# Optimization experiments

Hardware: AMD Instinct MI355X
Metric: run time of the kernel (lower is better)

The kernel has to match this reference:

```python
import jax, jax.numpy as jnp
import numpy as np


def setup_inputs() -> dict:
    key = jax.random.key(0)
    ks = jax.random.split(key, 8)
    B, N, H = 8, 64, 256
    nE, E = 256, 64
    HID, OUT = 512, 1
    s1 = 1.0 / np.sqrt(H + E)
    s2 = 1.0 / np.sqrt(HID)
    return {
        "h_all": jax.random.normal(ks[0], (B, N, H), dtype=jnp.float32),
        "e_feat": jax.random.normal(ks[1], (nE, E), dtype=jnp.float32),
        "W1": jax.random.normal(ks[2], (H + E, HID), dtype=jnp.float32) * s1,
        "b1": jnp.zeros((HID,), dtype=jnp.float32),
        "W2": jax.random.normal(ks[3], (HID, HID), dtype=jnp.float32) * s2,
        "b2": jnp.zeros((HID,), dtype=jnp.float32),
        "W3": jax.random.normal(ks[4], (HID, OUT), dtype=jnp.float32) * s2,
        "b3": jnp.zeros((OUT,), dtype=jnp.float32),
    }


def reference(h_all, e_feat, W1, b1, W2, b2, W3, b3):
    # Math == MLP(cat([expand(h), expand(e)], -1)) but computed via split
    # weights: cat([h,e]) @ W1 == h @ W1[:H] + e @ W1[H:], avoiding the
    # materialized [B,N,nE,H+E] concat tensor.
    H = h_all.shape[-1]
    Wh, We = W1[:H], W1[H:]
    h_part = jnp.einsum("bnh,hk->bnk", h_all, Wh)        # [B,N,HID]
    e_part = jnp.einsum("ed,dk->ek", e_feat, We)          # [nE,HID]
    x = h_part[:, :, None, :] + e_part[None, None, :, :] + b1  # [B,N,nE,HID]
    x = jax.nn.relu(x)
    x = jax.nn.relu(jnp.einsum("bnek,kj->bnej", x, W2) + b2)
    return jnp.einsum("bnek,ko->bneo", x, W3) + b3        # [B,N,nE,OUT]
```

## Files before the change

kernel.cpp:

```cpp
#include <hip/hip_runtime.h>
#include <hip/hip_bf16.h>
#include <hip/hip_fp16.h>


typedef __attribute__((ext_vector_type(8))) _Float16 f16x8;
typedef __attribute__((ext_vector_type(4))) float f32x4;

static __device__ __forceinline__ ushort2 pk_f16(float a, float b) {
  union { __half2 h; ushort2 u; } c;
  c.h = __float22half2_rn(make_float2(a, b));
  return c.u;
}

__global__ __launch_bounds__(256) void k_prep(
    const float* __restrict__ h_all, const float* __restrict__ e_feat,
    const float* __restrict__ W1, const float* __restrict__ b1,
    const float* __restrict__ W2,
    unsigned short* __restrict__ hpb, unsigned short* __restrict__ epb,
    unsigned short* __restrict__ w2f) {
  __shared__ float sm[64 * 68];
  const int t = threadIdx.x;
  const int b = blockIdx.x;

  if (b < 256) {
    const int r0 = b * 2;
    float (*hs)[256] = (float(*)[256])sm;
    hs[0][t] = h_all[(size_t)r0 * 256 + t];
    hs[1][t] = h_all[(size_t)(r0 + 1) * 256 + t];
    __syncthreads();
    float2 a0 = make_float2(0.f, 0.f), a1 = make_float2(0.f, 0.f);
    #pragma unroll 2
    for (int k = 0; k < 256; k += 4) {
      float2 w0 = *(const float2*)(W1 + (size_t)k * 512 + 2 * t);
      float2 w1 = *(const float2*)(W1 + (size_t)(k + 1) * 512 + 2 * t);
      float2 w2v = *(const float2*)(W1 + (size_t)(k + 2) * 512 + 2 * t);
      float2 w3v = *(const float2*)(W1 + (size_t)(k + 3) * 512 + 2 * t);
      float h00 = hs[0][k], h01 = hs[0][k + 1], h02 = hs[0][k + 2], h03 = hs[0][k + 3];
      float h10 = hs[1][k], h11 = hs[1][k + 1], h12 = hs[1][k + 2], h13 = hs[1][k + 3];
      a0.x = fmaf(h00, w0.x, a0.x); a0.y = fmaf(h00, w0.y, a0.y);
      a1.x = fmaf(h10, w0.x, a1.x); a1.y = fmaf(h10, w0.y, a1.y);
      a0.x = fmaf(h01, w1.x, a0.x); a0.y = fmaf(h01, w1.y, a0.y);
      a1.x = fmaf(h11, w1.x, a1.x); a1.y = fmaf(h11, w1.y, a1.y);
      a0.x = fmaf(h02, w2v.x, a0.x); a0.y = fmaf(h02, w2v.y, a0.y);
      a1.x = fmaf(h12, w2v.x, a1.x); a1.y = fmaf(h12, w2v.y, a1.y);
      a0.x = fmaf(h03, w3v.x, a0.x); a0.y = fmaf(h03, w3v.y, a0.y);
      a1.x = fmaf(h13, w3v.x, a1.x); a1.y = fmaf(h13, w3v.y, a1.y);
    }
    float2 bv = *(const float2*)(b1 + 2 * t);
    *(ushort2*)(hpb + (size_t)r0 * 512 + 2 * t) = pk_f16(a0.x + bv.x, a0.y + bv.y);
    *(ushort2*)(hpb + (size_t)(r0 + 1) * 512 + 2 * t) = pk_f16(a1.x + bv.x, a1.y + bv.y);
  } else if (b < 288) {
    const int r0 = (b - 256) * 8;
    sm[t] = e_feat[(size_t)r0 * 64 + t];
    sm[256 + t] = e_feat[(size_t)r0 * 64 + 256 + t];
    __syncthreads();
    float2 acc[8];
    #pragma unroll
    for (int i = 0; i < 8; ++i) acc[i] = make_float2(0.f, 0.f);
    for (int k = 0; k < 64; ++k) {
      float2 wv = *(const float2*)(W1 + (size_t)(256 + k) * 512 + 2 * t);
      #pragma unroll
      for (int i = 0; i < 8; ++i) {
        acc[i].x = fmaf(sm[i * 64 + k], wv.x, acc[i].x);
        acc[i].y = fmaf(sm[i * 64 + k], wv.y, acc[i].y);
      }
    }
    #pragma unroll
    for (int i = 0; i < 8; ++i)
      *(ushort2*)(epb + (size_t)(r0 + i) * 512 + 2 * t) = pk_f16(acc[i].x, acc[i].y);
  } else {
    const int bb = b - 288;
    const int k0 = (bb >> 3) * 64;
    const int c0 = (bb & 7) * 64;
    #pragma unroll
    for (int rr = 0; rr < 4; ++rr) {
      const int row = rr * 16 + (t >> 4);
      float4 v = *(const float4*)(W2 + (size_t)(k0 + row) * 512 + c0 + (t & 15) * 4);
      *(float4*)(&sm[row * 68 + (t & 15) * 4]) = v;
    }
    __syncthreads();
    #pragma unroll
    for (int s2 = 0; s2 < 2; ++s2) {
      const int s = t * 2 + s2;
      const int rec = s >> 6, l = s & 63;
      const int jg = (c0 >> 4) + (rec & 3);
      const int ksg = (k0 >> 5) + (rec >> 2);
      const int cl = (rec & 3) * 16 + (l & 15);
      const int kl = (rec >> 2) * 32 + (l >> 4) * 8;
      union { ushort2 o[4]; uint4 v; } u;
      #pragma unroll
      for (int uu = 0; uu < 4; ++uu)
        u.o[uu] = pk_f16(sm[(kl + 2 * uu) * 68 + cl], sm[(kl + 2 * uu + 1) * 68 + cl]);
      *(uint4*)(w2f + ((size_t)(jg * 16 + ksg) * 64 + l) * 8) = u.v;
    }
  }
}

__global__ __launch_bounds__(256, 2) void k_main(
    const unsigned short* __restrict__ hpb, const unsigned short* __restrict__ epb,
    const unsigned short* __restrict__ w2f, const float* __restrict__ b2,
    const float* __restrict__ W3, const float* __restrict__ b3,
    float* __restrict__ out) {
  __shared__ unsigned short x1s[64 * 512];

  const int t = threadIdx.x;
  const int lane = t & 63;
  const int w = t >> 6;
  const int l15 = lane & 15, l4 = lane >> 4;
  const int bn = blockIdx.x >> 2;
  const int e0 = (blockIdx.x & 3) << 6;
  const int off = (blockIdx.x * 11) & 15;
  const unsigned short* hprow = hpb + (size_t)bn * 512;

  const unsigned short* wrec = w2f + (size_t)w * 65536 + (size_t)lane * 8;
  f16x8 bb[2][8];
  #pragma unroll
  for (int j = 0; j < 8; ++j) {
    bb[0][j] = *(const f16x8*)(wrec + j * 8192 + (size_t)off * 512);
    bb[1][j] = *(const f16x8*)(wrec + j * 8192 + (size_t)((off + 1) & 15) * 512);
  }

  {
    const int kk = t & 63;
    const int rbase = t >> 6;
    const f16x8 fz = {0, 0, 0, 0, 0, 0, 0, 0};
    const f16x8 hv = *(const f16x8*)(hprow + kk * 8);
    #pragma unroll 2
    for (int rr = 0; rr < 16; ++rr) {
      const int r = rr * 4 + rbase;
      f16x8 ev = *(const f16x8*)(epb + (size_t)(e0 + r) * 512 + kk * 8);
      f16x8 x = hv + ev;
      x = __builtin_elementwise_max(x, fz);
      *(f16x8*)(&x1s[r * 512 + (kk ^ (r & 7)) * 8]) = x;
    }
  }
  __syncthreads();

  f32x4 acc[4][8] = {};
  #pragma unroll 2
  for (int ks = 0; ks < 14; ++ks) {
    const int cur = ks & 1;
    const int kr = (ks + off) & 15;
    const int krb = (ks + 2 + off) & 15;
    f16x8 a[4];
    #pragma unroll
    for (int i = 0; i < 4; ++i) {
      const int r = i * 16 + l15;
      a[i] = *(const f16x8*)(&x1s[r * 512 + (((kr * 4 + l4) ^ (l15 & 7)) * 8)]);
    }
    __builtin_amdgcn_s_setprio(1);
    #pragma unroll
    for (int i = 0; i < 4; ++i)
      #pragma unroll
      for (int j = 0; j < 8; ++j)
        acc[i][j] = __builtin_amdgcn_mfma_f32_16x16x32_f16(a[i], bb[cur][j], acc[i][j], 0, 0, 0);
    __builtin_amdgcn_s_setprio(0);
    #pragma unroll
    for (int j = 0; j < 8; ++j)
      bb[cur][j] = *(const f16x8*)(wrec + j * 8192 + (size_t)krb * 512);
  }
  #pragma unroll
  for (int ks = 14; ks < 16; ++ks) {
    const int cur = ks & 1;
    const int kr = (ks + off) & 15;
    f16x8 a[4];
    #pragma unroll
    for (int i = 0; i < 4; ++i) {
      const int r = i * 16 + l15;
      a[i] = *(const f16x8*)(&x1s[r * 512 + (((kr * 4 + l4) ^ (l15 & 7)) * 8)]);
    }
    __builtin_amdgcn_s_setprio(1);
    #pragma unroll
    for (int i = 0; i < 4; ++i)
      #pragma unroll
      for (int j = 0; j < 8; ++j)
        acc[i][j] = __builtin_amdgcn_mfma_f32_16x16x32_f16(a[i], bb[cur][j], acc[i][j], 0, 0, 0);
    __builtin_amdgcn_s_setprio(0);
  }

  float part[16];
  #pragma unroll
  for (int u = 0; u < 16; ++u) part[u] = 0.f;
  #pragma unroll
  for (int j = 0; j < 8; ++j) {
    const int n = w * 128 + j * 16 + l15;
    const float b2v = b2[n], w3v = W3[n];
    #pragma unroll
    for (int i = 0; i < 4; ++i)
      #pragma unroll
      for (int r = 0; r < 4; ++r)
        part[i * 4 + r] = fmaf(fmaxf(acc[i][j][r] + b2v, 0.f), w3v, part[i * 4 + r]);
  }
  #pragma unroll
  for (int u = 0; u < 16; ++u) {
    float v = part[u];
    v += __shfl_xor(v, 1);
    v += __shfl_xor(v, 2);
    v += __shfl_xor(v, 4);
    v += __shfl_xor(v, 8);
    part[u] = v;
  }
  __syncthreads();
  float* osum = (float*)x1s;
  if (l15 == 0) {
    #pragma unroll
    for (int i = 0; i < 4; ++i)
      #pragma unroll
      for (int r = 0; r < 4; ++r)
        osum[w * 64 + i * 16 + l4 * 4 + r] = part[i * 4 + r];
  }
  __syncthreads();
  if (t < 64) {
    float s = b3[0] + osum[t] + osum[64 + t] + osum[128 + t] + osum[192 + t];
    out[(size_t)bn * 256 + e0 + t] = s;
  }
}

extern "C" void kernel_launch(void* const* d_in, const int* in_sizes, int n_in,
                              void* d_out, int out_size, void* d_ws, size_t ws_size,
                              hipStream_t stream) {
  const float* h_all  = (const float*)d_in[0];
  const float* e_feat = (const float*)d_in[1];
  const float* W1     = (const float*)d_in[2];
  const float* b1     = (const float*)d_in[3];
  const float* W2     = (const float*)d_in[4];
  const float* b2     = (const float*)d_in[5];
  const float* W3     = (const float*)d_in[6];
  const float* b3     = (const float*)d_in[7];
  float* out = (float*)d_out;

  unsigned short* hpb = (unsigned short*)d_ws;
  unsigned short* epb = hpb + 512 * 512;
  unsigned short* w2f = epb + 256 * 512;

  hipLaunchKernelGGL(k_prep, dim3(352), dim3(256), 0, stream,
                     h_all, e_feat, W1, b1, W2, hpb, epb, w2f);
  hipLaunchKernelGGL(k_main, dim3(2048), dim3(256), 0, stream,
                     hpb, epb, w2f, b2, W3, b3, out);
}
```

Measured before the change: 140.7 us.

## Switch second-layer GEMM to 32x32x16 MFMA with matching W2 fragment layout

```diff
diff --git a/kernel.cpp b/kernel.cpp
--- a/kernel.cpp
+++ b/kernel.cpp
@@ -4,7 +4,7 @@
 
 
 typedef __attribute__((ext_vector_type(8))) _Float16 f16x8;
-typedef __attribute__((ext_vector_type(4))) float f32x4;
+typedef __attribute__((ext_vector_type(16))) float f32x16;
 
 static __device__ __forceinline__ ushort2 pk_f16(float a, float b) {
   union { __half2 h; ushort2 u; } c;
@@ -69,9 +69,9 @@
     for (int i = 0; i < 8; ++i)
       *(ushort2*)(epb + (size_t)(r0 + i) * 512 + 2 * t) = pk_f16(acc[i].x, acc[i].y);
   } else {
-    const int bb = b - 288;
-    const int k0 = (bb >> 3) * 64;
-    const int c0 = (bb & 7) * 64;
+    const int bbk = b - 288;
+    const int k0 = (bbk >> 3) * 64;
+    const int c0 = (bbk & 7) * 64;
     #pragma unroll
     for (int rr = 0; rr < 4; ++rr) {
       const int row = rr * 16 + (t >> 4);
@@ -83,15 +83,15 @@
     for (int s2 = 0; s2 < 2; ++s2) {
       const int s = t * 2 + s2;
       const int rec = s >> 6, l = s & 63;
-      const int jg = (c0 >> 4) + (rec & 3);
-      const int ksg = (k0 >> 5) + (rec >> 2);
-      const int cl = (rec & 3) * 16 + (l & 15);
-      const int kl = (rec >> 2) * 32 + (l >> 4) * 8;
+      const int jg = (c0 >> 5) + (rec & 1);
+      const int ks = (k0 >> 4) + (rec >> 1);
+      const int cl = (rec & 1) * 32 + (l & 31);
+      const int kl = (rec >> 1) * 16 + (l >> 5) * 8;
       union { ushort2 o[4]; uint4 v; } u;
       #pragma unroll
       for (int uu = 0; uu < 4; ++uu)
         u.o[uu] = pk_f16(sm[(kl + 2 * uu) * 68 + cl], sm[(kl + 2 * uu + 1) * 68 + cl]);
-      *(uint4*)(w2f + ((size_t)(jg * 16 + ksg) * 64 + l) * 8) = u.v;
+      *(uint4*)(w2f + ((size_t)(jg * 32 + ks) * 64 + l) * 8) = u.v;
     }
   }
 }
@@ -106,18 +106,18 @@
   const int t = threadIdx.x;
   const int lane = t & 63;
   const int w = t >> 6;
-  const int l15 = lane & 15, l4 = lane >> 4;
+  const int l31 = lane & 31, l5 = lane >> 5;
   const int bn = blockIdx.x >> 2;
   const int e0 = (blockIdx.x & 3) << 6;
-  const int off = (blockIdx.x * 11) & 15;
+  const int off = (blockIdx.x * 11) & 31;
   const unsigned short* hprow = hpb + (size_t)bn * 512;
 
   const unsigned short* wrec = w2f + (size_t)w * 65536 + (size_t)lane * 8;
-  f16x8 bb[2][8];
-  #pragma unroll
-  for (int j = 0; j < 8; ++j) {
-    bb[0][j] = *(const f16x8*)(wrec + j * 8192 + (size_t)off * 512);
-    bb[1][j] = *(const f16x8*)(wrec + j * 8192 + (size_t)((off + 1) & 15) * 512);
+  f16x8 bb[2][4];
+  #pragma unroll
+  for (int j = 0; j < 4; ++j) {
+    bb[0][j] = *(const f16x8*)(wrec + j * 16384 + (size_t)off * 512);
+    bb[1][j] = *(const f16x8*)(wrec + j * 16384 + (size_t)((off + 1) & 31) * 512);
   }
 
   {
@@ -131,83 +131,88 @@
       f16x8 ev = *(const f16x8*)(epb + (size_t)(e0 + r) * 512 + kk * 8);
       f16x8 x = hv + ev;
       x = __builtin_elementwise_max(x, fz);
-      *(f16x8*)(&x1s[r * 512 + (kk ^ (r & 7)) * 8]) = x;
+      *(f16x8*)(&x1s[r * 512 + ((kk ^ (r & 31)) * 8)]) = x;
     }
   }
   __syncthreads();
 
-  f32x4 acc[4][8] = {};
+  f32x16 acc[2][4] = {};
   #pragma unroll 2
-  for (int ks = 0; ks < 14; ++ks) {
+  for (int ks = 0; ks < 30; ++ks) {
     const int cur = ks & 1;
-    const int kr = (ks + off) & 15;
-    const int krb = (ks + 2 + off) & 15;
-    f16x8 a[4];
-    #pragma unroll
-    for (int i = 0; i < 4; ++i) {
-      const int r = i * 16 + l15;
-      a[i] = *(const f16x8*)(&x1s[r * 512 + (((kr * 4 + l4) ^ (l15 & 7)) * 8)]);
+    const int kr = (ks + off) & 31;
+    const int krb = (ks + 2 + off) & 31;
+    f16x8 a[2];
+    #pragma unroll
+    for (int i = 0; i < 2; ++i) {
+      const int r = i * 32 + l31;
+      a[i] = *(const f16x8*)(&x1s[r * 512 + (((kr * 2 + l5) ^ l31) * 8)]);
     }
     __builtin_amdgcn_s_setprio(1);
     #pragma unroll
-    for (int i = 0; i < 4; ++i)
-      #pragma unroll
-      for (int j = 0; j < 8; ++j)
-        acc[i][j] = __builtin_amdgcn_mfma_f32_16x16x32_f16(a[i], bb[cur][j], acc[i][j], 0, 0, 0);
+    for (int i = 0; i < 2; ++i)
+      #pragma unroll
+      for (int j = 0; j < 4; ++j)
+        acc[i][j] = __builtin_amdgcn_mfma_f32_32x32x16_f16(a[i], bb[cur][j], acc[i][j], 0, 0, 0);
     __builtin_amdgcn_s_setprio(0);
     #pragma unroll
-    for (int j = 0; j < 8; ++j)
-      bb[cur][j] = *(const f16x8*)(wrec + j * 8192 + (size_t)krb * 512);
-  }
-  #pragma unroll
-  for (int ks = 14; ks < 16; ++ks) {
+    for (int j = 0; j < 4; ++j)
+      bb[cur][j] = *(const f16x8*)(wrec + j * 16384 + (size_t)krb * 512);
+  }
+  #pragma unroll
+  for (int ks = 30; ks < 32; ++ks) {
     const int cur = ks & 1;
-    const int kr = (ks + off) & 15;
-    f16x8 a[4];
-    #pragma unroll
-    for (int i = 0; i < 4; ++i) {
-      const int r = i * 16 + l15;
-      a[i] = *(const f16x8*)(&x1s[r * 512 + (((kr * 4 + l4) ^ (l15 & 7)) * 8)]);
+    const int kr = (ks + off) & 31;
+    f16x8 a[2];
+    #pragma unroll
+    for (int i = 0; i < 2; ++i) {
+      const int r = i * 32 + l31;
+      a[i] = *(const f16x8*)(&x1s[r * 512 + (((kr * 2 + l5) ^ l31) * 8)]);
     }
     __builtin_amdgcn_s_setprio(1);
     #pragma unroll
-    for (int i = 0; i < 4; ++i)
-      #pragma unroll
-      for (int j = 0; j < 8; ++j)
-        acc[i][j] = __builtin_amdgcn_mfma_f32_16x16x32_f16(a[i], bb[cur][j], acc[i][j], 0, 0, 0);
+    for (int i = 0; i < 2; ++i)
+      #pragma unroll
+      for (int j = 0; j < 4; ++j)
+        acc[i][j] = __builtin_amdgcn_mfma_f32_32x32x16_f16(a[i], bb[cur][j], acc[i][j], 0, 0, 0);
     __builtin_amdgcn_s_setprio(0);
   }
 
-  float part[16];
-  #pragma unroll
-  for (int u = 0; u < 16; ++u) part[u] = 0.f;
-  #pragma unroll
-  for (int j = 0; j < 8; ++j) {
-    const int n = w * 128 + j * 16 + l15;
+  float part[2][16];
+  #pragma unroll
+  for (int i = 0; i < 2; ++i)
+    #pragma unroll
+    for (int r = 0; r < 16; ++r) part[i][r] = 0.f;
+  #pragma unroll
+  for (int j = 0; j < 4; ++j) {
+    const int n = w * 128 + j * 32 + l31;
     const float b2v = b2[n], w3v = W3[n];
     #pragma unroll
-    for (int i = 0; i < 4; ++i)
-      #pragma unroll
-      for (int r = 0; r < 4; ++r)
-        part[i * 4 + r] = fmaf(fmaxf(acc[i][j][r] + b2v, 0.f), w3v, part[i * 4 + r]);
-  }
-  #pragma unroll
-  for (int u = 0; u < 16; ++u) {
-    float v = part[u];
-    v += __shfl_xor(v, 1);
-    v += __shfl_xor(v, 2);
-    v += __shfl_xor(v, 4);
-    v += __shfl_xor(v, 8);
-    part[u] = v;
-  }
+    for (int i = 0; i < 2; ++i)
+      #pragma unroll
+      for (int r = 0; r < 16; ++r)
+        part[i][r] = fmaf(fmaxf(acc[i][j][r] + b2v, 0.f), w3v, part[i][r]);
+  }
+  #pragma unroll
+  for (int i = 0; i < 2; ++i)
+    #pragma unroll
+    for (int r = 0; r < 16; ++r) {
+      float v = part[i][r];
+      v += __shfl_xor(v, 1);
+      v += __shfl_xor(v, 2);
+      v += __shfl_xor(v, 4);
+      v += __shfl_xor(v, 8);
+      v += __shfl_xor(v, 16);
+      part[i][r] = v;
+    }
   __syncthreads();
   float* osum = (float*)x1s;
-  if (l15 == 0) {
-    #pragma unroll
-    for (int i = 0; i < 4; ++i)
-      #pragma unroll
-      for (int r = 0; r < 4; ++r)
-        osum[w * 64 + i * 16 + l4 * 4 + r] = part[i * 4 + r];
+  if (l31 == 0) {
+    #pragma unroll
+    for (int i = 0; i < 2; ++i)
+      #pragma unroll
+      for (int r = 0; r < 16; ++r)
+        osum[w * 64 + i * 32 + (r & 3) + 8 * (r >> 2) + 4 * l5] = part[i][r];
   }
   __syncthreads();
   if (t < 64) {
```

Result: slower. 159.2 us (+13.2%).
